# Performance work log

Hardware: AMD Instinct MI355X
Metric: run time of the kernel (lower is better)

Reference implementation:

```python
import jax, jax.numpy as jnp
import numpy as np

N_NODES = 100000
N_EDGES = 1600000
IN_DIM, HID_DIM, OUT_DIM = 256, 128, 64


def setup_inputs() -> dict:
    key = jax.random.key(0)
    k1, k2, k3, k4, k5 = jax.random.split(key, 5)
    h = jax.random.normal(k1, (N_NODES, IN_DIM), dtype=jnp.float32)
    src = jax.random.randint(k2, (N_EDGES,), 0, N_NODES, dtype=jnp.int32)
    dst = jax.random.randint(k3, (N_EDGES,), 0, N_NODES, dtype=jnp.int32)
    # Glorot-uniform weights like DGL GraphConv defaults, zero bias
    lim1 = np.sqrt(6.0 / (IN_DIM + HID_DIM))
    lim2 = np.sqrt(6.0 / (HID_DIM + OUT_DIM))
    W1 = jax.random.uniform(k4, (IN_DIM, HID_DIM), jnp.float32, -lim1, lim1)
    W2 = jax.random.uniform(k5, (HID_DIM, OUT_DIM), jnp.float32, -lim2, lim2)
    b1 = jnp.zeros((HID_DIM,), jnp.float32)
    b2 = jnp.zeros((OUT_DIM,), jnp.float32)
    return {"h": h, "W1": W1, "b1": b1, "W2": W2, "b2": b2, "src": src, "dst": dst}


def _graph_conv(h, W, b, src, dst):
    # DGL GraphConv, norm='both', allow_zero_in_degree=True:
    #   out = D_in^{-1/2} A D_out^{-1/2} h W + b  (degrees clamped to min 1)
    ones = jnp.ones(src.shape[0], dtype=h.dtype)
    deg_out = jnp.clip(jax.ops.segment_sum(ones, src, num_segments=N_NODES), 1.0, None)
    feat = h * (deg_out ** -0.5)[:, None]
    # in_feats > out_feats for both layers -> multiply by W first (DGL order)
    feat = feat @ W  # [N, out]
    agg = jax.ops.segment_sum(feat[src], dst, num_segments=N_NODES)  # SpMM
    deg_in = jnp.clip(jax.ops.segment_sum(ones, dst, num_segments=N_NODES), 1.0, None)
    return agg * (deg_in ** -0.5)[:, None] + b


def reference(h, W1, b1, W2, b2, src, dst):
    # dropout is identity in eval mode (training=False)
    x = _graph_conv(h, W1, b1, src, dst)
    x = jax.nn.relu(x)
    logits = _graph_conv(x, W2, b2, src, dst)
    return jax.nn.softmax(logits, axis=1), logits
```

## Files before the change

### kernel.cpp

```cpp
#include <hip/hip_runtime.h>
#include <cstdio>

#define NN 100000
#define NE 1600000
#define IN_DIM 256
#define HID_DIM 128
#define OUT_DIM 64

#define EPB 4096
#define NBLK ((NE + EPB - 1) / EPB)
#define FBSH 7
#define FBN 128
#define NFB 782
#define CAP 2560

typedef short s8v __attribute__((ext_vector_type(8)));
typedef float f4v __attribute__((ext_vector_type(4)));
typedef unsigned short u16x4 __attribute__((ext_vector_type(4)));
typedef unsigned short u16x8 __attribute__((ext_vector_type(8)));

__device__ __forceinline__ unsigned short f2bf(float f) {
    unsigned u = __builtin_bit_cast(unsigned, f);
    u += 0x7FFFu + ((u >> 16) & 1u);
    return (unsigned short)(u >> 16);
}
__device__ __forceinline__ float bf2f(unsigned short s) {
    unsigned u = ((unsigned)s) << 16;
    return __builtin_bit_cast(float, u);
}

__global__ __launch_bounds__(256) void scat1_kernel(const int* __restrict__ src,
                                                    const int* __restrict__ dst,
                                                    unsigned short* __restrict__ cnt2dD,
                                                    unsigned short* __restrict__ cnt2dS) {
    __shared__ unsigned hbD[NFB], hbS[NFB];
    const int t = threadIdx.x;
    for (int i = t; i < NFB; i += 256) { hbD[i] = 0u; hbS[i] = 0u; }
    __syncthreads();
    const int base = blockIdx.x * EPB;
    int n = NE - base; if (n > EPB) n = EPB;
    for (int i = t; i < n; i += 256) {
        atomicAdd(&hbD[dst[base + i] >> FBSH], 1u);
        atomicAdd(&hbS[src[base + i] >> FBSH], 1u);
    }
    __syncthreads();
    const size_t row = (size_t)blockIdx.x * NFB;
    for (int i = t; i < NFB; i += 256) {
        cnt2dD[row + i] = (unsigned short)hbD[i];
        cnt2dS[row + i] = (unsigned short)hbS[i];
    }
}

__global__ __launch_bounds__(128) void scanC_kernel(unsigned short* __restrict__ cnt2dD,
                                                    unsigned short* __restrict__ cnt2dS,
                                                    unsigned* __restrict__ btotD,
                                                    unsigned* __restrict__ btotS) {
    __shared__ unsigned sc[128];
    const int g = blockIdx.x;
    unsigned short* arr = (g < NFB) ? cnt2dD : cnt2dS;
    unsigned* btot = (g < NFB) ? btotD : btotS;
    const int b = (g < NFB) ? g : g - NFB;
    const int t = threadIdx.x;
    unsigned v[4];
    unsigned s = 0;
#pragma unroll
    for (int i = 0; i < 4; ++i) {
        int blk = t * 4 + i;
        unsigned x = (blk < NBLK) ? (unsigned)arr[(size_t)blk * NFB + b] : 0u;
        v[i] = s;
        s += x;
    }
    sc[t] = s;
    __syncthreads();
    for (int o = 1; o < 128; o <<= 1) {
        unsigned add = (t >= o) ? sc[t - o] : 0u;
        __syncthreads();
        sc[t] += add;
        __syncthreads();
    }
    unsigned incl = sc[t];
    unsigned excl = incl - s;
#pragma unroll
    for (int i = 0; i < 4; ++i) {
        int blk = t * 4 + i;
        if (blk < NBLK) arr[(size_t)blk * NFB + b] = (unsigned short)(excl + v[i]);
    }
    if (t == 127) btot[b] = incl;
}

__global__ __launch_bounds__(256) void scat2_kernel(const int* __restrict__ src,
                                                    const int* __restrict__ dst,
                                                    const unsigned short* __restrict__ ofsD,
                                                    const unsigned short* __restrict__ ofsS,
                                                    unsigned* __restrict__ ebufD,
                                                    unsigned char* __restrict__ ebufS) {
    __shared__ unsigned curD[NFB], curS[NFB];
    const int t = threadIdx.x;
    const size_t row = (size_t)blockIdx.x * NFB;
    for (int i = t; i < NFB; i += 256) {
        curD[i] = (unsigned)i * CAP + (unsigned)ofsD[row + i];
        curS[i] = (unsigned)i * CAP + (unsigned)ofsS[row + i];
    }
    __syncthreads();
    const int base = blockIdx.x * EPB;
    int n = NE - base; if (n > EPB) n = EPB;
    for (int i = t; i < n; i += 256) {
        int d = dst[base + i];
        int s = src[base + i];
        unsigned pD = atomicAdd(&curD[d >> FBSH], 1u);
        ebufD[pD] = ((unsigned)(d & 127) << 17) | (unsigned)s;
        unsigned pS = atomicAdd(&curS[s >> FBSH], 1u);
        ebufS[pS] = (unsigned char)(s & 127);
    }
}

__global__ __launch_bounds__(256) void bsort_kernel(const unsigned* __restrict__ ebufD,
                                                    const unsigned* __restrict__ btotD,
                                                    int* __restrict__ csr,
                                                    unsigned* __restrict__ rsinfo,
                                                    float* __restrict__ dsin) {
    __shared__ unsigned hn[FBN];
    __shared__ unsigned sc[FBN];
    __shared__ unsigned cur[FBN];
    const int b = blockIdx.x;
    const int t = threadIdx.x;
    const unsigned e0 = (unsigned)b * CAP;
    const unsigned e1 = e0 + btotD[b];
    if (t < FBN) hn[t] = 0u;
    __syncthreads();
    for (unsigned j = e0 + t; j < e1; j += 256) atomicAdd(&hn[(ebufD[j] >> 17) & 127u], 1u);
    __syncthreads();
    unsigned cnt_t = (t < FBN) ? hn[t] : 0u;
    if (t < FBN) sc[t] = cnt_t;
    __syncthreads();
    for (int o = 1; o < FBN; o <<= 1) {
        unsigned add = (t < FBN && t >= o) ? sc[t - o] : 0u;
        __syncthreads();
        if (t < FBN) sc[t] += add;
        __syncthreads();
    }
    if (t < FBN) {
        unsigned excl = sc[t] - cnt_t;
        cur[t] = e0 + excl;
        int node = (b << FBSH) + t;
        if (node < NN) {
            rsinfo[node] = ((e0 + excl) << 10) | (cnt_t & 1023u);
            dsin[node] = rsqrtf((float)(cnt_t ? cnt_t : 1u));
        }
    }
    __syncthreads();
    for (unsigned j = e0 + t; j < e1; j += 256) {
        unsigned pk = ebufD[j];
        unsigned pos = atomicAdd(&cur[(pk >> 17) & 127u], 1u);
        csr[pos] = (int)(pk & 0x1FFFFu);
    }
}

__global__ __launch_bounds__(256) void countB_kernel(const unsigned char* __restrict__ ebufS,
                                                     const unsigned* __restrict__ btotS,
                                                     unsigned* __restrict__ cnt_out) {
    __shared__ unsigned hist[FBN];
    const int b = blockIdx.x;
    const int t = threadIdx.x;
    if (t < FBN) hist[t] = 0u;
    __syncthreads();
    const unsigned n = btotS[b];
    const unsigned e0 = (unsigned)b * CAP;
    for (unsigned j = t; j < n; j += 256) atomicAdd(&hist[ebufS[e0 + j]], 1u);
    __syncthreads();
    if (t < FBN) {
        int node = (b << FBSH) + t;
        if (node < NN) cnt_out[node] = hist[t];
    }
}

__global__ __launch_bounds__(256) void prep_w_kernel(const float* __restrict__ W1,
                                                     const float* __restrict__ W2,
                                                     unsigned short* __restrict__ W1t,
                                                     unsigned short* __restrict__ W2t) {
    int i = blockIdx.x * 256 + threadIdx.x;
    if (i < HID_DIM * IN_DIM) {
        int n = i >> 8, k = i & 255;
        W1t[i] = f2bf(W1[k * HID_DIM + n]);
    } else if (i < HID_DIM * IN_DIM + OUT_DIM * HID_DIM) {
        int m = i - HID_DIM * IN_DIM;
        int n = m >> 7, k = m & 127;
        W2t[m] = f2bf(W2[k * OUT_DIM + n]);
    }
}

__global__ __launch_bounds__(256) void gemm1_kernel(const float* __restrict__ h,
                                                    const unsigned short* __restrict__ W1t,
                                                    const unsigned* __restrict__ cnt_out,
                                                    unsigned short* __restrict__ feat1, int M) {
    __shared__ unsigned short sA[128][56];
    __shared__ unsigned short sB[128][56];
    const int tid = threadIdx.x;
    const int lane = tid & 63;
    const int wave = tid >> 6;
    const int wm = wave >> 1, wn = wave & 1;
    const int m0 = blockIdx.x * 128;

    f4v acc[4][4];
#pragma unroll
    for (int i = 0; i < 4; ++i)
#pragma unroll
        for (int j = 0; j < 4; ++j) acc[i][j] = (f4v)0.f;

    const int arow = tid >> 3;
    const int akq = tid & 7;
    float sc[4];
#pragma unroll
    for (int i = 0; i < 4; ++i) {
        int m = m0 + arow + i * 32;
        if (m < M) {
            unsigned c = cnt_out[m];
            sc[i] = rsqrtf((float)(c ? c : 1u));
        } else sc[i] = 0.f;
    }

    for (int k0 = 0; k0 < IN_DIM; k0 += 32) {
#pragma unroll
        for (int i = 0; i < 4; ++i) {
            int row = arow + i * 32;
            int m = m0 + row;
            float4 v = make_float4(0.f, 0.f, 0.f, 0.f);
            if (m < M) v = *reinterpret_cast<const float4*>(&h[(size_t)m * IN_DIM + k0 + akq * 4]);
            u16x4 p;
            p[0] = f2bf(v.x * sc[i]);
            p[1] = f2bf(v.y * sc[i]);
            p[2] = f2bf(v.z * sc[i]);
            p[3] = f2bf(v.w * sc[i]);
            *reinterpret_cast<u16x4*>(&sA[row][akq * 4]) = p;
        }
#pragma unroll
        for (int i = 0; i < 2; ++i) {
            int idx = tid + i * 256;
            int row = idx >> 2, kq = idx & 3;
            u16x8 w = *reinterpret_cast<const u16x8*>(&W1t[(size_t)row * IN_DIM + k0 + kq * 8]);
            *reinterpret_cast<u16x8*>(&sB[row][kq * 8]) = w;
        }
        __syncthreads();
        s8v a[4];
#pragma unroll
        for (int mi = 0; mi < 4; ++mi)
            a[mi] = *reinterpret_cast<const s8v*>(&sA[wm * 64 + mi * 16 + (lane & 15)][(lane >> 4) * 8]);
#pragma unroll
        for (int ni = 0; ni < 4; ++ni) {
            s8v b = *reinterpret_cast<const s8v*>(&sB[wn * 64 + ni * 16 + (lane & 15)][(lane >> 4) * 8]);
#pragma unroll
            for (int mi = 0; mi < 4; ++mi)
                acc[mi][ni] = __builtin_amdgcn_mfma_f32_16x16x32_bf16(a[mi], b, acc[mi][ni], 0, 0, 0);
        }
        __syncthreads();
    }
#pragma unroll
    for (int mi = 0; mi < 4; ++mi)
#pragma unroll
        for (int ni = 0; ni < 4; ++ni) {
            int col = wn * 64 + ni * 16 + (lane & 15);
#pragma unroll
            for (int j = 0; j < 4; ++j) {
                int row = m0 + wm * 64 + mi * 16 + (lane >> 4) * 4 + j;
                if (row < M) feat1[(size_t)row * HID_DIM + col] = f2bf(acc[mi][ni][j]);
            }
        }
}

__global__ __launch_bounds__(256) void gemm2_kernel(const unsigned short* __restrict__ xs,
                                                    const unsigned short* __restrict__ W2t,
                                                    unsigned short* __restrict__ feat2, int M) {
    __shared__ unsigned short sA[128][56];
    __shared__ unsigned short sB[64][56];
    const int tid = threadIdx.x;
    const int lane = tid & 63;
    const int wave = tid >> 6;
    const int wm = wave >> 1, wn = wave & 1;
    const int m0 = blockIdx.x * 128;

    f4v acc[4][2];
#pragma unroll
    for (int i = 0; i < 4; ++i)
#pragma unroll
        for (int j = 0; j < 2; ++j) acc[i][j] = (f4v)0.f;

    for (int k0 = 0; k0 < HID_DIM; k0 += 32) {
#pragma unroll
        for (int i = 0; i < 2; ++i) {
            int idx = tid + i * 256;
            int row = idx >> 2, kq = idx & 3;
            int m = m0 + row;
            u16x8 w = (u16x8)0;
            if (m < M) w = *reinterpret_cast<const u16x8*>(&xs[(size_t)m * HID_DIM + k0 + kq * 8]);
            *reinterpret_cast<u16x8*>(&sA[row][kq * 8]) = w;
        }
        {
            int row = tid >> 2, kq = tid & 3;
            u16x8 w = *reinterpret_cast<const u16x8*>(&W2t[(size_t)row * HID_DIM + k0 + kq * 8]);
            *reinterpret_cast<u16x8*>(&sB[row][kq * 8]) = w;
        }
        __syncthreads();
        s8v a[4];
#pragma unroll
        for (int mi = 0; mi < 4; ++mi)
            a[mi] = *reinterpret_cast<const s8v*>(&sA[wm * 64 + mi * 16 + (lane & 15)][(lane >> 4) * 8]);
#pragma unroll
        for (int ni = 0; ni < 2; ++ni) {
            s8v b = *reinterpret_cast<const s8v*>(&sB[wn * 32 + ni * 16 + (lane & 15)][(lane >> 4) * 8]);
#pragma unroll
            for (int mi = 0; mi < 4; ++mi)
                acc[mi][ni] = __builtin_amdgcn_mfma_f32_16x16x32_bf16(a[mi], b, acc[mi][ni], 0, 0, 0);
        }
        __syncthreads();
    }
#pragma unroll
    for (int mi = 0; mi < 4; ++mi)
#pragma unroll
        for (int ni = 0; ni < 2; ++ni) {
            int col = wn * 32 + ni * 16 + (lane & 15);
#pragma unroll
            for (int j = 0; j < 4; ++j) {
                int row = m0 + wm * 64 + mi * 16 + (lane >> 4) * 4 + j;
                if (row < M) feat2[(size_t)row * OUT_DIM + col] = f2bf(acc[mi][ni][j]);
            }
        }
}

__global__ __launch_bounds__(256) void spmm1_kernel(const unsigned short* __restrict__ feat,
                                                    const int* __restrict__ csr,
                                                    const unsigned* __restrict__ rsinfo,
                                                    const float* __restrict__ dsin,
                                                    const unsigned* __restrict__ cnt_out,
                                                    const float* __restrict__ b1,
                                                    unsigned short* __restrict__ xs) {
    int wave = threadIdx.x >> 6;
    int lane = threadIdx.x & 63;
    int node = blockIdx.x * 4 + wave;
    if (node >= NN) return;
    unsigned info = rsinfo[node];
    unsigned j = info >> 10;
    int rem = (int)(info & 1023u);
    int c = lane * 2;
    float ax = 0.f, ay = 0.f;
    while (rem > 0) {
        int take = rem < 64 ? rem : 64;
        int idx = (lane < take) ? csr[j + lane] : 0;
        int e = 0;
        for (; e + 4 <= take; e += 4) {
            int s0 = __shfl(idx, e, 64);
            int s1 = __shfl(idx, e + 1, 64);
            int s2 = __shfl(idx, e + 2, 64);
            int s3 = __shfl(idx, e + 3, 64);
            unsigned v0 = *reinterpret_cast<const unsigned*>(&feat[(size_t)s0 * HID_DIM + c]);
            unsigned v1 = *reinterpret_cast<const unsigned*>(&feat[(size_t)s1 * HID_DIM + c]);
            unsigned v2 = *reinterpret_cast<const unsigned*>(&feat[(size_t)s2 * HID_DIM + c]);
            unsigned v3 = *reinterpret_cast<const unsigned*>(&feat[(size_t)s3 * HID_DIM + c]);
            ax += bf2f((unsigned short)(v0 & 0xffff)) + bf2f((unsigned short)(v1 & 0xffff))
                + bf2f((unsigned short)(v2 & 0xffff)) + bf2f((unsigned short)(v3 & 0xffff));
            ay += bf2f((unsigned short)(v0 >> 16)) + bf2f((unsigned short)(v1 >> 16))
                + bf2f((unsigned short)(v2 >> 16)) + bf2f((unsigned short)(v3 >> 16));
        }
        for (; e < take; ++e) {
            int s0 = __shfl(idx, e, 64);
            unsigned v0 = *reinterpret_cast<const unsigned*>(&feat[(size_t)s0 * HID_DIM + c]);
            ax += bf2f((unsigned short)(v0 & 0xffff));
            ay += bf2f((unsigned short)(v0 >> 16));
        }
        j += take; rem -= take;
    }
    float si = dsin[node];
    unsigned co = cnt_out[node];
    float so = rsqrtf((float)(co ? co : 1u));
    float2 bb = *reinterpret_cast<const float2*>(&b1[c]);
    float x0 = fmaxf(ax * si + bb.x, 0.f) * so;
    float x1 = fmaxf(ay * si + bb.y, 0.f) * so;
    unsigned p = ((unsigned)f2bf(x1) << 16) | (unsigned)f2bf(x0);
    *reinterpret_cast<unsigned*>(&xs[(size_t)node * HID_DIM + c]) = p;
}

__global__ __launch_bounds__(256) void spmm2_kernel(const unsigned short* __restrict__ feat2,
                                                    const int* __restrict__ csr,
                                                    const unsigned* __restrict__ rsinfo,
                                                    const float* __restrict__ dsin,
                                                    const float* __restrict__ b2,
                                                    float* __restrict__ out) {
    int wave = threadIdx.x >> 6;
    int lane = threadIdx.x & 63;
    int node = blockIdx.x * 4 + wave;
    if (node >= NN) return;
    unsigned info = rsinfo[node];
    unsigned j = info >> 10;
    int rem = (int)(info & 1023u);
    int half = lane >> 5;
    int c2 = (lane & 31) * 2;
    float a0 = 0.f, a1 = 0.f;
    while (rem > 0) {
        int take = rem < 64 ? rem : 64;
        int idx = (lane < take) ? csr[j + lane] : 0;
        int e = 0;
        for (; e + 8 <= take; e += 8) {
            int sA = __shfl(idx, e + half, 64);
            int sB = __shfl(idx, e + 2 + half, 64);
            int sC = __shfl(idx, e + 4 + half, 64);
            int sD = __shfl(idx, e + 6 + half, 64);
            unsigned vA = *reinterpret_cast<const unsigned*>(&feat2[(size_t)sA * OUT_DIM + c2]);
            unsigned vB = *reinterpret_cast<const unsigned*>(&feat2[(size_t)sB * OUT_DIM + c2]);
            unsigned vC = *reinterpret_cast<const unsigned*>(&feat2[(size_t)sC * OUT_DIM + c2]);
            unsigned vD = *reinterpret_cast<const unsigned*>(&feat2[(size_t)sD * OUT_DIM + c2]);
            a0 += bf2f((unsigned short)(vA & 0xffff)) + bf2f((unsigned short)(vB & 0xffff))
                + bf2f((unsigned short)(vC & 0xffff)) + bf2f((unsigned short)(vD & 0xffff));
            a1 += bf2f((unsigned short)(vA >> 16)) + bf2f((unsigned short)(vB >> 16))
                + bf2f((unsigned short)(vC >> 16)) + bf2f((unsigned short)(vD >> 16));
        }
        for (; e + 2 <= take; e += 2) {
            int sA = __shfl(idx, e + half, 64);
            unsigned vA = *reinterpret_cast<const unsigned*>(&feat2[(size_t)sA * OUT_DIM + c2]);
            a0 += bf2f((unsigned short)(vA & 0xffff));
            a1 += bf2f((unsigned short)(vA >> 16));
        }
        if (e < take) {
            int sA = __shfl(idx, e, 64);
            if (half == 0) {
                unsigned vA = *reinterpret_cast<const unsigned*>(&feat2[(size_t)sA * OUT_DIM + c2]);
                a0 += bf2f((unsigned short)(vA & 0xffff));
                a1 += bf2f((unsigned short)(vA >> 16));
            }
        }
        j += take; rem -= take;
    }
    a0 += __shfl_xor(a0, 32, 64);
    a1 += __shfl_xor(a1, 32, 64);
    float si = dsin[node];
    float2 bb = *reinterpret_cast<const float2*>(&b2[c2]);
    float l0 = a0 * si + bb.x;
    float l1 = a1 * si + bb.y;
    float m = fmaxf(l0, l1);
    for (int o = 16; o > 0; o >>= 1) m = fmaxf(m, __shfl_xor(m, o, 64));
    float e0 = __expf(l0 - m), e1 = __expf(l1 - m);
    float s = e0 + e1;
    for (int o = 16; o > 0; o >>= 1) s += __shfl_xor(s, o, 64);
    float inv = 1.0f / s;
    if (half == 0) {
        *reinterpret_cast<float2*>(&out[(size_t)node * OUT_DIM + c2]) =
            make_float2(e0 * inv, e1 * inv);
        *reinterpret_cast<float2*>(&out[(size_t)NN * OUT_DIM + (size_t)node * OUT_DIM + c2]) =
            make_float2(l0, l1);
    }
}

static inline size_t align_up(size_t x, size_t a) { return (x + a - 1) & ~(a - 1); }

extern "C" void kernel_launch(void* const* d_in, const int* in_sizes, int n_in,
                              void* d_out, int out_size, void* d_ws, size_t ws_size,
                              hipStream_t stream) {
    (void)in_sizes; (void)n_in; (void)out_size;
    const float* h = (const float*)d_in[0];
    const float* W1 = (const float*)d_in[1];
    const float* b1 = (const float*)d_in[2];
    const float* W2 = (const float*)d_in[3];
    const float* b2 = (const float*)d_in[4];
    const int* src = (const int*)d_in[5];
    const int* dst = (const int*)d_in[6];
    float* out = (float*)d_out;

    char* ws = (char*)d_ws;
    size_t off = 0;
    auto alloc = [&](size_t bytes) {
        void* p = (void*)(ws + off);
        off = align_up(off + bytes, 512);
        return p;
    };
    unsigned* cnt_out = (unsigned*)alloc(NN * 4);
    unsigned short* cnt2dD = (unsigned short*)alloc((size_t)NBLK * NFB * 2);
    unsigned short* cnt2dS = (unsigned short*)alloc((size_t)NBLK * NFB * 2);
    unsigned* btotD = (unsigned*)alloc(NFB * 4);
    unsigned* btotS = (unsigned*)alloc(NFB * 4);
    unsigned* rsinfo = (unsigned*)alloc(NN * 4);
    float* dsin = (float*)alloc(NN * 4);
    unsigned* ebufD = (unsigned*)alloc((size_t)NFB * CAP * 4);
    unsigned char* ebufS = (unsigned char*)alloc((size_t)NFB * CAP);
    int* csr = (int*)alloc((size_t)NFB * CAP * 4);
    unsigned short* W1t = (unsigned short*)alloc((size_t)HID_DIM * IN_DIM * 2);
    unsigned short* W2t = (unsigned short*)alloc((size_t)OUT_DIM * HID_DIM * 2);
    unsigned short* feat1 = (unsigned short*)alloc((size_t)NN * HID_DIM * 2);
    unsigned short* xs = (unsigned short*)alloc((size_t)NN * HID_DIM * 2);
    unsigned short* feat2 = feat1;

    if (off > ws_size) {
        fprintf(stderr, "kernel_launch: ws too small: need %zu, have %zu\n", off, ws_size);
        return;
    }

    prep_w_kernel<<<(HID_DIM * IN_DIM + OUT_DIM * HID_DIM + 255) / 256, 256, 0, stream>>>(
        W1, W2, W1t, W2t);

    scat1_kernel<<<NBLK, 256, 0, stream>>>(src, dst, cnt2dD, cnt2dS);
    scanC_kernel<<<2 * NFB, 128, 0, stream>>>(cnt2dD, cnt2dS, btotD, btotS);
    scat2_kernel<<<NBLK, 256, 0, stream>>>(src, dst, cnt2dD, cnt2dS, ebufD, ebufS);
    bsort_kernel<<<NFB, 256, 0, stream>>>(ebufD, btotD, csr, rsinfo, dsin);
    countB_kernel<<<NFB, 256, 0, stream>>>(ebufS, btotS, cnt_out);

    gemm1_kernel<<<(NN + 127) / 128, 256, 0, stream>>>(h, W1t, cnt_out, feat1, NN);
    spmm1_kernel<<<(NN + 3) / 4, 256, 0, stream>>>(feat1, csr, rsinfo, dsin, cnt_out, b1, xs);
    gemm2_kernel<<<(NN + 127) / 128, 256, 0, stream>>>(xs, W2t, feat2, NN);
    spmm2_kernel<<<(NN + 3) / 4, 256, 0, stream>>>(feat2, csr, rsinfo, dsin, b2, out);
}
```

Before: 241.5 us.

## Double-buffer GEMM A tiles, load weights directly, move degree scaling to epilogue

Both dense GEMM kernels now double-buffer the A tile in shared memory, prefetching the next K-slice into registers while MFMAs run on the current one. This leaves one barrier per step instead of two. The weight B fragments are read straight from global memory (small, cache-resident) instead of being staged through LDS, and the LDS row stride shrinks. In gemm1 the out-degree rsqrt scaling moves from the A-load path to the epilogue. That removes per-element multiplies in the loop, but it changes where bf16 rounding happens.

```diff
diff --git a/kernel.cpp b/kernel.cpp
--- a/kernel.cpp
+++ b/kernel.cpp
@@ -193,85 +193,99 @@
                                                     const unsigned short* __restrict__ W1t,
                                                     const unsigned* __restrict__ cnt_out,
                                                     unsigned short* __restrict__ feat1, int M) {
-    __shared__ unsigned short sA[128][56];
-    __shared__ unsigned short sB[128][56];
+    __shared__ unsigned short sA[2][128][40];
     const int tid = threadIdx.x;
     const int lane = tid & 63;
     const int wave = tid >> 6;
     const int wm = wave >> 1, wn = wave & 1;
     const int m0 = blockIdx.x * 128;
-
-    f4v acc[4][4];
-#pragma unroll
-    for (int i = 0; i < 4; ++i)
-#pragma unroll
-        for (int j = 0; j < 4; ++j) acc[i][j] = (f4v)0.f;
-
     const int arow = tid >> 3;
     const int akq = tid & 7;
-    float sc[4];
+
+    f4v acc[4][4];
+#pragma unroll
+    for (int i = 0; i < 4; ++i)
+#pragma unroll
+        for (int j = 0; j < 4; ++j) acc[i][j] = (f4v)0.f;
+
+    int mrow[4]; bool mok[4];
+#pragma unroll
+    for (int i = 0; i < 4; ++i) { mrow[i] = m0 + arow + i * 32; mok[i] = mrow[i] < M; }
+
+    float4 pre[4];
+#pragma unroll
+    for (int i = 0; i < 4; ++i)
+        pre[i] = mok[i] ? *reinterpret_cast<const float4*>(&h[(size_t)mrow[i] * IN_DIM + akq * 4])
+                        : make_float4(0.f, 0.f, 0.f, 0.f);
 #pragma unroll
     for (int i = 0; i < 4; ++i) {
-        int m = m0 + arow + i * 32;
-        if (m < M) {
-            unsigned c = cnt_out[m];
-            sc[i] = rsqrtf((float)(c ? c : 1u));
-        } else sc[i] = 0.f;
-    }
-
-    for (int k0 = 0; k0 < IN_DIM; k0 += 32) {
-#pragma unroll
-        for (int i = 0; i < 4; ++i) {
-            int row = arow + i * 32;
-            int m = m0 + row;
-            float4 v = make_float4(0.f, 0.f, 0.f, 0.f);
-            if (m < M) v = *reinterpret_cast<const float4*>(&h[(size_t)m * IN_DIM + k0 + akq * 4]);
-            u16x4 p;
-            p[0] = f2bf(v.x * sc[i]);
-            p[1] = f2bf(v.y * sc[i]);
-            p[2] = f2bf(v.z * sc[i]);
-            p[3] = f2bf(v.w * sc[i]);
-            *reinterpret_cast<u16x4*>(&sA[row][akq * 4]) = p;
-        }
-#pragma unroll
-        for (int i = 0; i < 2; ++i) {
-            int idx = tid + i * 256;
-            int row = idx >> 2, kq = idx & 3;
-            u16x8 w = *reinterpret_cast<const u16x8*>(&W1t[(size_t)row * IN_DIM + k0 + kq * 8]);
-            *reinterpret_cast<u16x8*>(&sB[row][kq * 8]) = w;
+        u16x4 p;
+        p[0] = f2bf(pre[i].x); p[1] = f2bf(pre[i].y);
+        p[2] = f2bf(pre[i].z); p[3] = f2bf(pre[i].w);
+        *reinterpret_cast<u16x4*>(&sA[0][arow + i * 32][akq * 4]) = p;
+    }
+    __syncthreads();
+
+    int cur = 0;
+#pragma unroll
+    for (int ks = 0; ks < 8; ++ks) {
+        if (ks < 7) {
+            const int k0n = (ks + 1) * 32;
+#pragma unroll
+            for (int i = 0; i < 4; ++i)
+                pre[i] = mok[i] ? *reinterpret_cast<const float4*>(
+                                      &h[(size_t)mrow[i] * IN_DIM + k0n + akq * 4])
+                                : make_float4(0.f, 0.f, 0.f, 0.f);
+        }
+        s8v bfrag[4];
+#pragma unroll
+        for (int ni = 0; ni < 4; ++ni)
+            bfrag[ni] = *reinterpret_cast<const s8v*>(
+                &W1t[(size_t)(wn * 64 + ni * 16 + (lane & 15)) * IN_DIM + ks * 32 + (lane >> 4) * 8]);
+        s8v afrag[4];
+#pragma unroll
+        for (int mi = 0; mi < 4; ++mi)
+            afrag[mi] = *reinterpret_cast<const s8v*>(
+                &sA[cur][wm * 64 + mi * 16 + (lane & 15)][(lane >> 4) * 8]);
+#pragma unroll
+        for (int ni = 0; ni < 4; ++ni)
+#pragma unroll
+            for (int mi = 0; mi < 4; ++mi)
+                acc[mi][ni] = __builtin_amdgcn_mfma_f32_16x16x32_bf16(afrag[mi], bfrag[ni], acc[mi][ni], 0, 0, 0);
+        if (ks < 7) {
+#pragma unroll
+            for (int i = 0; i < 4; ++i) {
+                u16x4 p;
+                p[0] = f2bf(pre[i].x); p[1] = f2bf(pre[i].y);
+                p[2] = f2bf(pre[i].z); p[3] = f2bf(pre[i].w);
+                *reinterpret_cast<u16x4*>(&sA[cur ^ 1][arow + i * 32][akq * 4]) = p;
+            }
         }
         __syncthreads();
-        s8v a[4];
-#pragma unroll
-        for (int mi = 0; mi < 4; ++mi)
-            a[mi] = *reinterpret_cast<const s8v*>(&sA[wm * 64 + mi * 16 + (lane & 15)][(lane >> 4) * 8]);
-#pragma unroll
-        for (int ni = 0; ni < 4; ++ni) {
-            s8v b = *reinterpret_cast<const s8v*>(&sB[wn * 64 + ni * 16 + (lane & 15)][(lane >> 4) * 8]);
-#pragma unroll
-            for (int mi = 0; mi < 4; ++mi)
-                acc[mi][ni] = __builtin_amdgcn_mfma_f32_16x16x32_bf16(a[mi], b, acc[mi][ni], 0, 0, 0);
-        }
-        __syncthreads();
-    }
-#pragma unroll
-    for (int mi = 0; mi < 4; ++mi)
-#pragma unroll
-        for (int ni = 0; ni < 4; ++ni) {
-            int col = wn * 64 + ni * 16 + (lane & 15);
-#pragma unroll
-            for (int j = 0; j < 4; ++j) {
-                int row = m0 + wm * 64 + mi * 16 + (lane >> 4) * 4 + j;
-                if (row < M) feat1[(size_t)row * HID_DIM + col] = f2bf(acc[mi][ni][j]);
+        cur ^= 1;
+    }
+#pragma unroll
+    for (int mi = 0; mi < 4; ++mi) {
+#pragma unroll
+        for (int j = 0; j < 4; ++j) {
+            int row = m0 + wm * 64 + mi * 16 + (lane >> 4) * 4 + j;
+            if (row < M) {
+                unsigned cdeg = cnt_out[row];
+                float s = rsqrtf((float)(cdeg ? cdeg : 1u));
+#pragma unroll
+                for (int ni = 0; ni < 4; ++ni) {
+                    int col = wn * 64 + ni * 16 + (lane & 15);
+                    feat1[(size_t)row * HID_DIM + col] = f2bf(acc[mi][ni][j] * s);
+                }
             }
         }
+    }
 }
 
 __global__ __launch_bounds__(256) void gemm2_kernel(const unsigned short* __restrict__ xs,
                                                     const unsigned short* __restrict__ W2t,
                                                     unsigned short* __restrict__ feat2, int M) {
-    __shared__ unsigned short sA[128][56];
-    __shared__ unsigned short sB[64][56];
+    __shared__ unsigned short sA[2][128][40];
     const int tid = threadIdx.x;
     const int lane = tid & 63;
     const int wave = tid >> 6;
@@ -284,34 +298,58 @@
 #pragma unroll
         for (int j = 0; j < 2; ++j) acc[i][j] = (f4v)0.f;
 
-    for (int k0 = 0; k0 < HID_DIM; k0 += 32) {
-#pragma unroll
-        for (int i = 0; i < 2; ++i) {
-            int idx = tid + i * 256;
-            int row = idx >> 2, kq = idx & 3;
-            int m = m0 + row;
-            u16x8 w = (u16x8)0;
-            if (m < M) w = *reinterpret_cast<const u16x8*>(&xs[(size_t)m * HID_DIM + k0 + kq * 8]);
-            *reinterpret_cast<u16x8*>(&sA[row][kq * 8]) = w;
-        }
-        {
-            int row = tid >> 2, kq = tid & 3;
-            u16x8 w = *reinterpret_cast<const u16x8*>(&W2t[(size_t)row * HID_DIM + k0 + kq * 8]);
-            *reinterpret_cast<u16x8*>(&sB[row][kq * 8]) = w;
+    int srow[2], skq[2]; bool sok[2];
+#pragma unroll
+    for (int i = 0; i < 2; ++i) {
+        int idx = tid + i * 256;
+        srow[i] = idx >> 2; skq[i] = idx & 3;
+        sok[i] = (m0 + srow[i]) < M;
+    }
+
+    u16x8 pre[2];
+#pragma unroll
+    for (int i = 0; i < 2; ++i)
+        pre[i] = sok[i] ? *reinterpret_cast<const u16x8*>(
+                              &xs[(size_t)(m0 + srow[i]) * HID_DIM + skq[i] * 8])
+                        : (u16x8)0;
+#pragma unroll
+    for (int i = 0; i < 2; ++i)
+        *reinterpret_cast<u16x8*>(&sA[0][srow[i]][skq[i] * 8]) = pre[i];
+    __syncthreads();
+
+    int cur = 0;
+#pragma unroll
+    for (int ks = 0; ks < 4; ++ks) {
+        if (ks < 3) {
+            const int k0n = (ks + 1) * 32;
+#pragma unroll
+            for (int i = 0; i < 2; ++i)
+                pre[i] = sok[i] ? *reinterpret_cast<const u16x8*>(
+                                      &xs[(size_t)(m0 + srow[i]) * HID_DIM + k0n + skq[i] * 8])
+                                : (u16x8)0;
+        }
+        s8v bfrag[2];
+#pragma unroll
+        for (int ni = 0; ni < 2; ++ni)
+            bfrag[ni] = *reinterpret_cast<const s8v*>(
+                &W2t[(size_t)(wn * 32 + ni * 16 + (lane & 15)) * HID_DIM + ks * 32 + (lane >> 4) * 8]);
+        s8v afrag[4];
+#pragma unroll
+        for (int mi = 0; mi < 4; ++mi)
+            afrag[mi] = *reinterpret_cast<const s8v*>(
+                &sA[cur][wm * 64 + mi * 16 + (lane & 15)][(lane >> 4) * 8]);
+#pragma unroll
+        for (int ni = 0; ni < 2; ++ni)
+#pragma unroll
+            for (int mi = 0; mi < 4; ++mi)
+                acc[mi][ni] = __builtin_amdgcn_mfma_f32_16x16x32_bf16(afrag[mi], bfrag[ni], acc[mi][ni], 0, 0, 0);
+        if (ks < 3) {
+#pragma unroll
+            for (int i = 0; i < 2; ++i)
+                *reinterpret_cast<u16x8*>(&sA[cur ^ 1][srow[i]][skq[i] * 8]) = pre[i];
         }
         __syncthreads();
-        s8v a[4];
-#pragma unroll
-        for (int mi = 0; mi < 4; ++mi)
-            a[mi] = *reinterpret_cast<const s8v*>(&sA[wm * 64 + mi * 16 + (lane & 15)][(lane >> 4) * 8]);
-#pragma unroll
-        for (int ni = 0; ni < 2; ++ni) {
-            s8v b = *reinterpret_cast<const s8v*>(&sB[wn * 32 + ni * 16 + (lane & 15)][(lane >> 4) * 8]);
-#pragma unroll
-            for (int mi = 0; mi < 4; ++mi)
-                acc[mi][ni] = __builtin_amdgcn_mfma_f32_16x16x32_bf16(a[mi], b, acc[mi][ni], 0, 0, 0);
-        }
-        __syncthreads();
+        cur ^= 1;
     }
 #pragma unroll
     for (int mi = 0; mi < 4; ++mi)
```

Result: faster. 236.7 us (-2.0%).
